# Kernel optimization log

Hardware: AMD Instinct MI355X
Metric: run time of the kernel (lower is better)

## Reference

```python
import jax, jax.numpy as jnp
import numpy as np

B, C, H, W = 16, 64, 128, 128
E = 8          # number of experts
TOPK = 2       # num_expert (top-k routing)


def setup_inputs() -> dict:
    key = jax.random.key(0)
    ks = jax.random.split(key, 8)
    s = 1.0 / np.sqrt(C)
    x = jax.random.normal(ks[0], (B, C, H, W), dtype=jnp.float32)
    k = jax.random.normal(ks[1], (B, C, 1, 1), dtype=jnp.float32)
    Wg = jax.random.normal(ks[2], (C, E), dtype=jnp.float32) * s
    bg = jnp.zeros((E,), dtype=jnp.float32)
    W1 = jax.random.normal(ks[3], (E, C, C), dtype=jnp.float32) * s  # [E, out, in]
    b1 = jnp.zeros((E, C), dtype=jnp.float32)
    W2 = jax.random.normal(ks[4], (E, C, C), dtype=jnp.float32) * s
    b2 = jnp.zeros((E, C), dtype=jnp.float32)
    return {"x": x, "k": k, "Wg": Wg, "bg": bg, "W1": W1, "b1": b1, "W2": W2, "b2": b2}


def reference(x, k, Wg, bg, W1, b1, W2, b2):
    # --- gate: global avg pool + linear -> [B, E] logits ---
    pooled = x.mean(axis=(2, 3))                              # [B, C]
    logits = pooled @ Wg + bg                                  # [B, E]
    # softmax in fp32 then cast back (matches F.softmax(dtype=torch.float).to(x.dtype))
    weights = jax.nn.softmax(logits.astype(jnp.float32), axis=1).astype(x.dtype)
    topk_w, topk_idx = jax.lax.top_k(weights, TOPK)           # [B, TOPK]
    # scatter top-k weights into dense per-expert mask [B, E]
    mask = jnp.zeros_like(weights).at[jnp.arange(B)[:, None], topk_idx].set(topk_w)
    # --- training branch: run ALL experts, combine with mask ---
    # expert_e(x, k) = W2_e @ gelu((W1_e @ x + b1_e) * k) + b2_e   (1x1 convs)
    h = jnp.einsum('eoc,bchw->ebohw', W1, x) + b1[:, None, :, None, None]
    h = jax.nn.gelu(h * k[None])                               # [E, B, C, H, W]
    y = jnp.einsum('eoc,ebchw->ebohw', W2, h) + b2[:, None, :, None, None]
    out = x + jnp.einsum('ebchw,be->bchw', y, mask)
    return out
```

## Files before the change

kernel.cpp:

```cpp
#include <hip/hip_runtime.h>
#include <hip/hip_bf16.h>


#define BB 16
#define CC 64
#define EE 8
#define HWPX 16384

typedef __bf16 bf16x8 __attribute__((ext_vector_type(8)));
typedef float f32x4 __attribute__((ext_vector_type(4)));

__device__ __forceinline__ unsigned packbf2(float lo, float hi) {
    __bf16 a = (__bf16)lo, b = (__bf16)hi;
    unsigned short ua = __builtin_bit_cast(unsigned short, a);
    unsigned short ub = __builtin_bit_cast(unsigned short, b);
    return ((unsigned)ub << 16) | (unsigned)ua;
}

__device__ __forceinline__ int swz(int px, int d) {
    return px * 32 + ((d & ~3) ^ ((px & 7) << 2)) + (d & 3);
}

__global__ __launch_bounds__(256) void pool_conv_kernel(
    const float* __restrict__ x, float* __restrict__ pooled,
    const float* __restrict__ W1, const float* __restrict__ W2,
    __bf16* __restrict__ W1b, __bf16* __restrict__ W2b) {
    int blk = blockIdx.x;
    if (blk < BB * CC) {
        const float4* p = (const float4*)(x + (size_t)blk * HWPX);
        float s = 0.f;
        for (int i = threadIdx.x; i < HWPX / 4; i += 256) {
            float4 v = p[i];
            s += (v.x + v.y) + (v.z + v.w);
        }
        #pragma unroll
        for (int off = 32; off > 0; off >>= 1) s += __shfl_down(s, off);
        __shared__ float ls[4];
        if ((threadIdx.x & 63) == 0) ls[threadIdx.x >> 6] = s;
        __syncthreads();
        if (threadIdx.x == 0) pooled[blk] = ((ls[0] + ls[1]) + (ls[2] + ls[3])) * (1.0f / (float)HWPX);
    } else {
        int i = (blk - BB * CC) * 256 + threadIdx.x;
        W1b[i] = (__bf16)W1[i];
        W2b[i] = (__bf16)W2[i];
    }
}

__global__ void gate_kernel(const float* __restrict__ pooled,
                            const float* __restrict__ Wg,
                            const float* __restrict__ bg,
                            int* __restrict__ gidx, float* __restrict__ gw) {
    int b = threadIdx.x;
    if (b >= BB) return;
    float logits[EE];
    #pragma unroll
    for (int e = 0; e < EE; ++e) logits[e] = bg[e];
    for (int c = 0; c < CC; ++c) {
        float pv = pooled[b * CC + c];
        #pragma unroll
        for (int e = 0; e < EE; ++e) logits[e] = fmaf(pv, Wg[c * EE + e], logits[e]);
    }
    float m = logits[0];
    #pragma unroll
    for (int e = 1; e < EE; ++e) m = fmaxf(m, logits[e]);
    float w[EE]; float den = 0.f;
    #pragma unroll
    for (int e = 0; e < EE; ++e) { w[e] = expf(logits[e] - m); den += w[e]; }
    float inv = 1.0f / den;
    #pragma unroll
    for (int e = 0; e < EE; ++e) w[e] *= inv;
    int i0 = 0;
    #pragma unroll
    for (int e = 1; e < EE; ++e) if (w[e] > w[i0]) i0 = e;
    int i1 = -1;
    #pragma unroll
    for (int e = 0; e < EE; ++e) {
        if (e == i0) continue;
        if (i1 < 0 || w[e] > w[i1]) i1 = e;
    }
    gidx[b * 2 + 0] = i0; gidx[b * 2 + 1] = i1;
    gw[b * 2 + 0] = w[i0]; gw[b * 2 + 1] = w[i1];
}

__global__ __launch_bounds__(256) void moe_main(
    const float* __restrict__ x, const float* __restrict__ kvec,
    const __bf16* __restrict__ W1b, const float* __restrict__ b1,
    const __bf16* __restrict__ W2b, const float* __restrict__ b2,
    const int* __restrict__ gidx, const float* __restrict__ gw,
    float* __restrict__ out) {

    __shared__ unsigned int LX[64 * 32];
    __shared__ unsigned int LH0[64 * 32];
    __shared__ unsigned int LH1[64 * 32];

    const int blk = blockIdx.x;
    const int b = blk >> 8;
    const int P0 = (blk & 255) << 6;
    const int t = threadIdx.x;
    const int w = t >> 6;
    const int l = t & 63;
    const int g = l >> 4;
    const int l15 = l & 15;

    const int arow = 16 * w + l15;
    const int r0w = 16 * w + 4 * g;
    const int d0 = 8 * w + 2 * g;

    const int e0 = __builtin_amdgcn_readfirstlane(gidx[b * 2 + 0]);
    const int e1 = __builtin_amdgcn_readfirstlane(gidx[b * 2 + 1]);
    const float wgt0 = gw[b * 2 + 0];
    const float wgt1 = gw[b * 2 + 1];

    bf16x8 a1f[2][2], a2f[2][2];
    #pragma unroll
    for (int ks = 0; ks < 2; ++ks) {
        a1f[0][ks] = *(const bf16x8*)(W1b + e0 * CC * CC + arow * CC + ks * 32 + g * 8);
        a1f[1][ks] = *(const bf16x8*)(W1b + e1 * CC * CC + arow * CC + ks * 32 + g * 8);
        a2f[0][ks] = *(const bf16x8*)(W2b + e0 * CC * CC + arow * CC + ks * 32 + g * 8);
        a2f[1][ks] = *(const bf16x8*)(W2b + e1 * CC * CC + arow * CC + ks * 32 + g * 8);
    }
    const f32x4 b1v0 = *(const f32x4*)(b1 + e0 * CC + r0w);
    const f32x4 b1v1 = *(const f32x4*)(b1 + e1 * CC + r0w);
    const f32x4 b2v0 = *(const f32x4*)(b2 + e0 * CC + r0w);
    const f32x4 b2v1 = *(const f32x4*)(b2 + e1 * CC + r0w);
    const f32x4 kk   = *(const f32x4*)(kvec + b * CC + r0w);
    float bsum[4];
    #pragma unroll
    for (int j = 0; j < 4; ++j) bsum[j] = fmaf(wgt0, b2v0[j], wgt1 * b2v1[j]);

    const float* xb = x + b * CC * HWPX;
    const int obase = r0w * HWPX + P0 + l15;
    float xc[16];
    #pragma unroll
    for (int cb = 0; cb < 4; ++cb)
        #pragma unroll
        for (int j = 0; j < 4; ++j)
            xc[cb * 4 + j] = xb[obase + j * HWPX + cb * 16];

    #pragma unroll
    for (int cb = 0; cb < 4; ++cb) {
        uint2 pk;
        pk.x = packbf2(xc[cb * 4 + 0], xc[cb * 4 + 1]);
        pk.y = packbf2(xc[cb * 4 + 2], xc[cb * 4 + 3]);
        *(uint2*)&LX[swz(cb * 16 + l15, d0)] = pk;
    }
    __syncthreads();

    f32x4 h0[4], h1[4];
    #pragma unroll
    for (int cb = 0; cb < 4; ++cb) {
        bf16x8 bx0 = *(const bf16x8*)&LX[swz(cb * 16 + l15, g * 4)];
        bf16x8 bx1 = *(const bf16x8*)&LX[swz(cb * 16 + l15, 16 + g * 4)];
        h0[cb] = (f32x4){0.f, 0.f, 0.f, 0.f};
        h1[cb] = (f32x4){0.f, 0.f, 0.f, 0.f};
        h0[cb] = __builtin_amdgcn_mfma_f32_16x16x32_bf16(a1f[0][0], bx0, h0[cb], 0, 0, 0);
        h0[cb] = __builtin_amdgcn_mfma_f32_16x16x32_bf16(a1f[0][1], bx1, h0[cb], 0, 0, 0);
        h1[cb] = __builtin_amdgcn_mfma_f32_16x16x32_bf16(a1f[1][0], bx0, h1[cb], 0, 0, 0);
        h1[cb] = __builtin_amdgcn_mfma_f32_16x16x32_bf16(a1f[1][1], bx1, h1[cb], 0, 0, 0);
    }

    const float C1 = -2.302208239f;
    const float C2 = -0.1029434f;

    #pragma unroll
    for (int cb = 0; cb < 4; ++cb) {
        float hv0[4], hv1[4];
        #pragma unroll
        for (int j = 0; j < 4; ++j) {
            float t0 = (h0[cb][j] + b1v0[j]) * kk[j];
            float ex0 = __builtin_amdgcn_exp2f(t0 * fmaf(C2, t0 * t0, C1));
            hv0[j] = (t0 * wgt0) * __builtin_amdgcn_rcpf(ex0 + 1.f);
            float t1 = (h1[cb][j] + b1v1[j]) * kk[j];
            float ex1 = __builtin_amdgcn_exp2f(t1 * fmaf(C2, t1 * t1, C1));
            hv1[j] = (t1 * wgt1) * __builtin_amdgcn_rcpf(ex1 + 1.f);
        }
        uint2 pk0, pk1;
        pk0.x = packbf2(hv0[0], hv0[1]);
        pk0.y = packbf2(hv0[2], hv0[3]);
        pk1.x = packbf2(hv1[0], hv1[1]);
        pk1.y = packbf2(hv1[2], hv1[3]);
        *(uint2*)&LH0[swz(cb * 16 + l15, d0)] = pk0;
        *(uint2*)&LH1[swz(cb * 16 + l15, d0)] = pk1;
    }
    __syncthreads();

    f32x4 acc[4];
    #pragma unroll
    for (int cb = 0; cb < 4; ++cb) {
        acc[cb] = (f32x4){0.f, 0.f, 0.f, 0.f};
        #pragma unroll
        for (int ks = 0; ks < 2; ++ks) {
            bf16x8 bh0 = *(const bf16x8*)&LH0[swz(cb * 16 + l15, ks * 16 + g * 4)];
            acc[cb] = __builtin_amdgcn_mfma_f32_16x16x32_bf16(a2f[0][ks], bh0, acc[cb], 0, 0, 0);
            bf16x8 bh1 = *(const bf16x8*)&LH1[swz(cb * 16 + l15, ks * 16 + g * 4)];
            acc[cb] = __builtin_amdgcn_mfma_f32_16x16x32_bf16(a2f[1][ks], bh1, acc[cb], 0, 0, 0);
        }
    }

    float* ob = out + b * CC * HWPX;
    #pragma unroll
    for (int cb = 0; cb < 4; ++cb)
        #pragma unroll
        for (int j = 0; j < 4; ++j)
            ob[obase + j * HWPX + cb * 16] = xc[cb * 4 + j] + (acc[cb][j] + bsum[j]);
}

extern "C" void kernel_launch(void* const* d_in, const int* in_sizes, int n_in,
                              void* d_out, int out_size, void* d_ws, size_t ws_size,
                              hipStream_t stream) {
    const float* x  = (const float*)d_in[0];
    const float* k  = (const float*)d_in[1];
    const float* Wg = (const float*)d_in[2];
    const float* bg = (const float*)d_in[3];
    const float* W1 = (const float*)d_in[4];
    const float* b1 = (const float*)d_in[5];
    const float* W2 = (const float*)d_in[6];
    const float* b2 = (const float*)d_in[7];
    float* out = (float*)d_out;

    float*  pooled = (float*)d_ws;
    int*    gidx   = (int*)((char*)d_ws + 4096);
    float*  gw     = (float*)((char*)d_ws + 4096 + 128);
    __bf16* W1b    = (__bf16*)((char*)d_ws + 8192);
    __bf16* W2b    = (__bf16*)((char*)d_ws + 8192 + 65536);

    pool_conv_kernel<<<BB * CC + EE * CC * CC / 256, 256, 0, stream>>>(x, pooled, W1, W2, W1b, W2b);
    gate_kernel<<<1, 64, 0, stream>>>(pooled, Wg, bg, gidx, gw);
    moe_main<<<BB * 256, 256, 0, stream>>>(x, k, W1b, b1, W2b, b2, gidx, gw, out);
}
```

Baseline: 51.55 us.

## Fuse gate into main MoE kernel and serialize experts to cut registers and LDS

```diff
diff --git a/kernel.cpp b/kernel.cpp
--- a/kernel.cpp
+++ b/kernel.cpp
@@ -46,52 +46,17 @@
     }
 }
 
-__global__ void gate_kernel(const float* __restrict__ pooled,
-                            const float* __restrict__ Wg,
-                            const float* __restrict__ bg,
-                            int* __restrict__ gidx, float* __restrict__ gw) {
-    int b = threadIdx.x;
-    if (b >= BB) return;
-    float logits[EE];
-    #pragma unroll
-    for (int e = 0; e < EE; ++e) logits[e] = bg[e];
-    for (int c = 0; c < CC; ++c) {
-        float pv = pooled[b * CC + c];
-        #pragma unroll
-        for (int e = 0; e < EE; ++e) logits[e] = fmaf(pv, Wg[c * EE + e], logits[e]);
-    }
-    float m = logits[0];
-    #pragma unroll
-    for (int e = 1; e < EE; ++e) m = fmaxf(m, logits[e]);
-    float w[EE]; float den = 0.f;
-    #pragma unroll
-    for (int e = 0; e < EE; ++e) { w[e] = expf(logits[e] - m); den += w[e]; }
-    float inv = 1.0f / den;
-    #pragma unroll
-    for (int e = 0; e < EE; ++e) w[e] *= inv;
-    int i0 = 0;
-    #pragma unroll
-    for (int e = 1; e < EE; ++e) if (w[e] > w[i0]) i0 = e;
-    int i1 = -1;
-    #pragma unroll
-    for (int e = 0; e < EE; ++e) {
-        if (e == i0) continue;
-        if (i1 < 0 || w[e] > w[i1]) i1 = e;
-    }
-    gidx[b * 2 + 0] = i0; gidx[b * 2 + 1] = i1;
-    gw[b * 2 + 0] = w[i0]; gw[b * 2 + 1] = w[i1];
-}
-
-__global__ __launch_bounds__(256) void moe_main(
+__global__ __launch_bounds__(256, 4) void moe_main(
     const float* __restrict__ x, const float* __restrict__ kvec,
+    const float* __restrict__ pooled, const float* __restrict__ Wg,
+    const float* __restrict__ bg,
     const __bf16* __restrict__ W1b, const float* __restrict__ b1,
     const __bf16* __restrict__ W2b, const float* __restrict__ b2,
-    const int* __restrict__ gidx, const float* __restrict__ gw,
     float* __restrict__ out) {
 
     __shared__ unsigned int LX[64 * 32];
     __shared__ unsigned int LH0[64 * 32];
-    __shared__ unsigned int LH1[64 * 32];
+    __shared__ unsigned int gateLds[4];
 
     const int blk = blockIdx.x;
     const int b = blk >> 8;
@@ -106,28 +71,6 @@
     const int r0w = 16 * w + 4 * g;
     const int d0 = 8 * w + 2 * g;
 
-    const int e0 = __builtin_amdgcn_readfirstlane(gidx[b * 2 + 0]);
-    const int e1 = __builtin_amdgcn_readfirstlane(gidx[b * 2 + 1]);
-    const float wgt0 = gw[b * 2 + 0];
-    const float wgt1 = gw[b * 2 + 1];
-
-    bf16x8 a1f[2][2], a2f[2][2];
-    #pragma unroll
-    for (int ks = 0; ks < 2; ++ks) {
-        a1f[0][ks] = *(const bf16x8*)(W1b + e0 * CC * CC + arow * CC + ks * 32 + g * 8);
-        a1f[1][ks] = *(const bf16x8*)(W1b + e1 * CC * CC + arow * CC + ks * 32 + g * 8);
-        a2f[0][ks] = *(const bf16x8*)(W2b + e0 * CC * CC + arow * CC + ks * 32 + g * 8);
-        a2f[1][ks] = *(const bf16x8*)(W2b + e1 * CC * CC + arow * CC + ks * 32 + g * 8);
-    }
-    const f32x4 b1v0 = *(const f32x4*)(b1 + e0 * CC + r0w);
-    const f32x4 b1v1 = *(const f32x4*)(b1 + e1 * CC + r0w);
-    const f32x4 b2v0 = *(const f32x4*)(b2 + e0 * CC + r0w);
-    const f32x4 b2v1 = *(const f32x4*)(b2 + e1 * CC + r0w);
-    const f32x4 kk   = *(const f32x4*)(kvec + b * CC + r0w);
-    float bsum[4];
-    #pragma unroll
-    for (int j = 0; j < 4; ++j) bsum[j] = fmaf(wgt0, b2v0[j], wgt1 * b2v1[j]);
-
     const float* xb = x + b * CC * HWPX;
     const int obase = r0w * HWPX + P0 + l15;
     float xc[16];
@@ -136,6 +79,44 @@
         #pragma unroll
         for (int j = 0; j < 4; ++j)
             xc[cb * 4 + j] = xb[obase + j * HWPX + cb * 16];
+
+    if (w == 0) {
+        float pv = pooled[b * CC + l];
+        f32x4 wgA = *(const f32x4*)(Wg + l * EE);
+        f32x4 wgB = *(const f32x4*)(Wg + l * EE + 4);
+        float le[EE] = {pv * wgA[0], pv * wgA[1], pv * wgA[2], pv * wgA[3],
+                        pv * wgB[0], pv * wgB[1], pv * wgB[2], pv * wgB[3]};
+        #pragma unroll
+        for (int mask = 1; mask < 64; mask <<= 1)
+            #pragma unroll
+            for (int e = 0; e < EE; ++e) le[e] += __shfl_xor(le[e], mask);
+        if (l == 0) {
+            float lg[EE];
+            float m = -1e30f;
+            #pragma unroll
+            for (int e = 0; e < EE; ++e) { lg[e] = le[e] + bg[e]; m = fmaxf(m, lg[e]); }
+            float den = 0.f;
+            #pragma unroll
+            for (int e = 0; e < EE; ++e) { lg[e] = expf(lg[e] - m); den += lg[e]; }
+            float inv = 1.0f / den;
+            float m0 = lg[0] * inv; int i0 = 0;
+            #pragma unroll
+            for (int e = 1; e < EE; ++e) {
+                float v = lg[e] * inv;
+                if (v > m0) { m0 = v; i0 = e; }
+            }
+            float m1 = -1.f; int i1 = 0;
+            #pragma unroll
+            for (int e = 0; e < EE; ++e) {
+                float v = lg[e] * inv;
+                if (e != i0 && v > m1) { m1 = v; i1 = e; }
+            }
+            gateLds[0] = (unsigned)i0;
+            gateLds[1] = (unsigned)i1;
+            gateLds[2] = __builtin_bit_cast(unsigned, m0);
+            gateLds[3] = __builtin_bit_cast(unsigned, m1);
+        }
+    }
 
     #pragma unroll
     for (int cb = 0; cb < 4; ++cb) {
@@ -146,55 +127,104 @@
     }
     __syncthreads();
 
-    f32x4 h0[4], h1[4];
+    const int e0 = __builtin_amdgcn_readfirstlane((int)gateLds[0]);
+    const int e1 = __builtin_amdgcn_readfirstlane((int)gateLds[1]);
+    const float wgt0 = __builtin_bit_cast(float, gateLds[2]);
+    const float wgt1 = __builtin_bit_cast(float, gateLds[3]);
+
+    const float C1 = -2.302208239f;
+    const float C2 = -0.1029434f;
+
+    const f32x4 kk = *(const f32x4*)(kvec + b * CC + r0w);
+
+    bf16x8 a1k0 = *(const bf16x8*)(W1b + e0 * CC * CC + arow * CC + g * 8);
+    bf16x8 a1k1 = *(const bf16x8*)(W1b + e0 * CC * CC + arow * CC + 32 + g * 8);
+    const f32x4 b1v0 = *(const f32x4*)(b1 + e0 * CC + r0w);
+    f32x4 h[4];
     #pragma unroll
     for (int cb = 0; cb < 4; ++cb) {
         bf16x8 bx0 = *(const bf16x8*)&LX[swz(cb * 16 + l15, g * 4)];
         bf16x8 bx1 = *(const bf16x8*)&LX[swz(cb * 16 + l15, 16 + g * 4)];
-        h0[cb] = (f32x4){0.f, 0.f, 0.f, 0.f};
-        h1[cb] = (f32x4){0.f, 0.f, 0.f, 0.f};
-        h0[cb] = __builtin_amdgcn_mfma_f32_16x16x32_bf16(a1f[0][0], bx0, h0[cb], 0, 0, 0);
-        h0[cb] = __builtin_amdgcn_mfma_f32_16x16x32_bf16(a1f[0][1], bx1, h0[cb], 0, 0, 0);
-        h1[cb] = __builtin_amdgcn_mfma_f32_16x16x32_bf16(a1f[1][0], bx0, h1[cb], 0, 0, 0);
-        h1[cb] = __builtin_amdgcn_mfma_f32_16x16x32_bf16(a1f[1][1], bx1, h1[cb], 0, 0, 0);
-    }
-
-    const float C1 = -2.302208239f;
-    const float C2 = -0.1029434f;
-
-    #pragma unroll
-    for (int cb = 0; cb < 4; ++cb) {
-        float hv0[4], hv1[4];
+        h[cb] = (f32x4){0.f, 0.f, 0.f, 0.f};
+        h[cb] = __builtin_amdgcn_mfma_f32_16x16x32_bf16(a1k0, bx0, h[cb], 0, 0, 0);
+        h[cb] = __builtin_amdgcn_mfma_f32_16x16x32_bf16(a1k1, bx1, h[cb], 0, 0, 0);
+    }
+    uint2 pk0[4];
+    #pragma unroll
+    for (int cb = 0; cb < 4; ++cb) {
+        float hv[4];
         #pragma unroll
         for (int j = 0; j < 4; ++j) {
-            float t0 = (h0[cb][j] + b1v0[j]) * kk[j];
-            float ex0 = __builtin_amdgcn_exp2f(t0 * fmaf(C2, t0 * t0, C1));
-            hv0[j] = (t0 * wgt0) * __builtin_amdgcn_rcpf(ex0 + 1.f);
-            float t1 = (h1[cb][j] + b1v1[j]) * kk[j];
-            float ex1 = __builtin_amdgcn_exp2f(t1 * fmaf(C2, t1 * t1, C1));
-            hv1[j] = (t1 * wgt1) * __builtin_amdgcn_rcpf(ex1 + 1.f);
-        }
-        uint2 pk0, pk1;
-        pk0.x = packbf2(hv0[0], hv0[1]);
-        pk0.y = packbf2(hv0[2], hv0[3]);
-        pk1.x = packbf2(hv1[0], hv1[1]);
-        pk1.y = packbf2(hv1[2], hv1[3]);
-        *(uint2*)&LH0[swz(cb * 16 + l15, d0)] = pk0;
-        *(uint2*)&LH1[swz(cb * 16 + l15, d0)] = pk1;
-    }
+            float t0 = (h[cb][j] + b1v0[j]) * kk[j];
+            float ex = __builtin_amdgcn_exp2f(t0 * fmaf(C2, t0 * t0, C1));
+            hv[j] = (t0 * wgt0) * __builtin_amdgcn_rcpf(ex + 1.f);
+        }
+        pk0[cb].x = packbf2(hv[0], hv[1]);
+        pk0[cb].y = packbf2(hv[2], hv[3]);
+    }
+
+    a1k0 = *(const bf16x8*)(W1b + e1 * CC * CC + arow * CC + g * 8);
+    a1k1 = *(const bf16x8*)(W1b + e1 * CC * CC + arow * CC + 32 + g * 8);
+    const f32x4 b1v1 = *(const f32x4*)(b1 + e1 * CC + r0w);
+    #pragma unroll
+    for (int cb = 0; cb < 4; ++cb) {
+        bf16x8 bx0 = *(const bf16x8*)&LX[swz(cb * 16 + l15, g * 4)];
+        bf16x8 bx1 = *(const bf16x8*)&LX[swz(cb * 16 + l15, 16 + g * 4)];
+        h[cb] = (f32x4){0.f, 0.f, 0.f, 0.f};
+        h[cb] = __builtin_amdgcn_mfma_f32_16x16x32_bf16(a1k0, bx0, h[cb], 0, 0, 0);
+        h[cb] = __builtin_amdgcn_mfma_f32_16x16x32_bf16(a1k1, bx1, h[cb], 0, 0, 0);
+    }
+    uint2 pk1[4];
+    #pragma unroll
+    for (int cb = 0; cb < 4; ++cb) {
+        float hv[4];
+        #pragma unroll
+        for (int j = 0; j < 4; ++j) {
+            float t1 = (h[cb][j] + b1v1[j]) * kk[j];
+            float ex = __builtin_amdgcn_exp2f(t1 * fmaf(C2, t1 * t1, C1));
+            hv[j] = (t1 * wgt1) * __builtin_amdgcn_rcpf(ex + 1.f);
+        }
+        pk1[cb].x = packbf2(hv[0], hv[1]);
+        pk1[cb].y = packbf2(hv[2], hv[3]);
+    }
+
+    #pragma unroll
+    for (int cb = 0; cb < 4; ++cb)
+        *(uint2*)&LH0[swz(cb * 16 + l15, d0)] = pk0[cb];
+
+    bf16x8 a2e0k0 = *(const bf16x8*)(W2b + e0 * CC * CC + arow * CC + g * 8);
+    bf16x8 a2e0k1 = *(const bf16x8*)(W2b + e0 * CC * CC + arow * CC + 32 + g * 8);
+    bf16x8 a2e1k0 = *(const bf16x8*)(W2b + e1 * CC * CC + arow * CC + g * 8);
+    bf16x8 a2e1k1 = *(const bf16x8*)(W2b + e1 * CC * CC + arow * CC + 32 + g * 8);
+    const f32x4 b2v0 = *(const f32x4*)(b2 + e0 * CC + r0w);
+    const f32x4 b2v1 = *(const f32x4*)(b2 + e1 * CC + r0w);
+    float bsum[4];
+    #pragma unroll
+    for (int j = 0; j < 4; ++j) bsum[j] = fmaf(wgt0, b2v0[j], wgt1 * b2v1[j]);
+
     __syncthreads();
 
+    #pragma unroll
+    for (int cb = 0; cb < 4; ++cb)
+        *(uint2*)&LX[swz(cb * 16 + l15, d0)] = pk1[cb];
+
     f32x4 acc[4];
     #pragma unroll
     for (int cb = 0; cb < 4; ++cb) {
         acc[cb] = (f32x4){0.f, 0.f, 0.f, 0.f};
-        #pragma unroll
-        for (int ks = 0; ks < 2; ++ks) {
-            bf16x8 bh0 = *(const bf16x8*)&LH0[swz(cb * 16 + l15, ks * 16 + g * 4)];
-            acc[cb] = __builtin_amdgcn_mfma_f32_16x16x32_bf16(a2f[0][ks], bh0, acc[cb], 0, 0, 0);
-            bf16x8 bh1 = *(const bf16x8*)&LH1[swz(cb * 16 + l15, ks * 16 + g * 4)];
-            acc[cb] = __builtin_amdgcn_mfma_f32_16x16x32_bf16(a2f[1][ks], bh1, acc[cb], 0, 0, 0);
-        }
+        bf16x8 bh0 = *(const bf16x8*)&LH0[swz(cb * 16 + l15, g * 4)];
+        bf16x8 bh1 = *(const bf16x8*)&LH0[swz(cb * 16 + l15, 16 + g * 4)];
+        acc[cb] = __builtin_amdgcn_mfma_f32_16x16x32_bf16(a2e0k0, bh0, acc[cb], 0, 0, 0);
+        acc[cb] = __builtin_amdgcn_mfma_f32_16x16x32_bf16(a2e0k1, bh1, acc[cb], 0, 0, 0);
+    }
+    __syncthreads();
+
+    #pragma unroll
+    for (int cb = 0; cb < 4; ++cb) {
+        bf16x8 bh0 = *(const bf16x8*)&LX[swz(cb * 16 + l15, g * 4)];
+        bf16x8 bh1 = *(const bf16x8*)&LX[swz(cb * 16 + l15, 16 + g * 4)];
+        acc[cb] = __builtin_amdgcn_mfma_f32_16x16x32_bf16(a2e1k0, bh0, acc[cb], 0, 0, 0);
+        acc[cb] = __builtin_amdgcn_mfma_f32_16x16x32_bf16(a2e1k1, bh1, acc[cb], 0, 0, 0);
     }
 
     float* ob = out + b * CC * HWPX;
@@ -219,12 +249,9 @@
     float* out = (float*)d_out;
 
     float*  pooled = (float*)d_ws;
-    int*    gidx   = (int*)((char*)d_ws + 4096);
-    float*  gw     = (float*)((char*)d_ws + 4096 + 128);
     __bf16* W1b    = (__bf16*)((char*)d_ws + 8192);
     __bf16* W2b    = (__bf16*)((char*)d_ws + 8192 + 65536);
 
     pool_conv_kernel<<<BB * CC + EE * CC * CC / 256, 256, 0, stream>>>(x, pooled, W1, W2, W1b, W2b);
-    gate_kernel<<<1, 64, 0, stream>>>(pooled, Wg, bg, gidx, gw);
-    moe_main<<<BB * 256, 256, 0, stream>>>(x, k, W1b, b1, W2b, b2, gidx, gw, out);
-}
+    moe_main<<<BB * 256, 256, 0, stream>>>(x, k, pooled, Wg, bg, W1b, b1, W2b, b2, out);
+}
```

After: 53.02 us. +2.8%, slower.
